# Kernel optimization log

Hardware: AMD Instinct MI355X
Metric: run time of the kernel (lower is better)

Reference implementation:

```python
import jax, jax.numpy as jnp
import numpy as np


def setup_inputs() -> dict:
    key = jax.random.key(0)
    ks = jax.random.split(key, 9)
    B, S, F = 16, 512, 1024
    scale = 1.0 / np.sqrt(2 * F)  # ~torch Linear init scale
    return {
        "v": jax.random.normal(ks[0], (B, S, F), jnp.float32),
        "t": jax.random.normal(ks[1], (B, S, F), jnp.float32),
        "a": jax.random.normal(ks[2], (B, S, F), jnp.float32),
        "W_tv": jax.random.normal(ks[3], (2 * F, F), jnp.float32) * scale,
        "b_tv": jnp.zeros((F,), jnp.float32),
        "W_ta": jax.random.normal(ks[4], (2 * F, F), jnp.float32) * scale,
        "b_ta": jnp.zeros((F,), jnp.float32),
        "W_av": jax.random.normal(ks[5], (2 * F, F), jnp.float32) * scale,
        "b_av": jnp.zeros((F,), jnp.float32),
    }


def _branch_feat(x1, x2, W, b):
    # tanh(Linear(cat(x1, x2)))  -- split weight to avoid materializing concat
    F = x1.shape[-1]
    W1, W2 = W[:F], W[F:]
    return jnp.tanh(jnp.einsum("bsf,fg->bsg", x1, W1)
                    + jnp.einsum("bsf,fg->bsg", x2, W2) + b)


def _attend_gate(q, feat):
    # softmax(q @ feat^T) @ q, gated by feat
    scores = jnp.einsum("bqf,bkf->bqk", q, feat)  # [B,S,S]
    p = jax.nn.softmax(scores, axis=-1)
    return jnp.einsum("bqk,bkf->bqf", p, q) * feat


def reference(v, t, a, W_tv, b_tv, W_ta, b_ta, W_av, b_av):
    Ftv = _branch_feat(t, v, W_tv, b_tv)
    Fta = _branch_feat(t, a, W_ta, b_ta)
    Fav = _branch_feat(a, v, W_av, b_av)
    Oatv = _attend_gate(a, Ftv)
    Ovta = _attend_gate(v, Fta)
    Otav = _attend_gate(t, Fav)
    return jnp.concatenate((Oatv, Ovta, Otav), axis=2)
```

## Files before the change

kernel.cpp:

```cpp
#include <hip/hip_runtime.h>

typedef unsigned short ushort_t;
typedef _Float16 f16x8 __attribute__((ext_vector_type(8)));
typedef float f32x4 __attribute__((ext_vector_type(4)));
typedef unsigned short u16x8 __attribute__((ext_vector_type(8)));

#define DEVINL __device__ __forceinline__

constexpr int B = 16, S = 512, F = 1024;
constexpr int M_ROWS = B * S;
constexpr size_t NX = (size_t)M_ROWS * F;
constexpr size_t NW = (size_t)F * (2 * F);

DEVINL ushort_t f2h(float f) { return __builtin_bit_cast(ushort_t, (_Float16)f); }
DEVINL float h2f(ushort_t h) { return (float)__builtin_bit_cast(_Float16, h); }

DEVINL void gload_lds16(const void* g, void* l) {
  __builtin_amdgcn_global_load_lds(
      (__attribute__((address_space(1))) void*)(g),
      (__attribute__((address_space(3))) void*)(l), 16, 0, 0);
}

DEVINL f32x4 mfma16h(f16x8 a, f16x8 b, f32x4 c) {
  return __builtin_amdgcn_mfma_f32_16x16x32_f16(a, b, c, 0, 0, 0);
}

template <int KSTEPS, int SPLIT_STEP>
DEVINL void gemm2p_core(const ushort_t* __restrict__ a1, const ushort_t* __restrict__ a2,
                        int lda, const ushort_t* __restrict__ bsrc, int ldb,
                        ushort_t* lds, int tid, f32x4 (&acc)[4][4]) {
  constexpr int BUF = 24576;
  constexpr int BOFF = 16384;
  constexpr int KM = KSTEPS - 1;
  const int lane = tid & 63, w = tid >> 6;
  const int wr = (w >> 1) * 64, wc = (w & 1) * 64;
  const int slog = (lane & 7) ^ ((lane >> 3) & 7);

  const int sl0 = ((lane >> 4) ^ (lane & 7)) * 8;
  const int sl1 = ((4 + (lane >> 4)) ^ (lane & 7)) * 8;
  const ushort_t* dsA0 = lds + (wr + (lane & 15)) * 64 + sl0;
  const ushort_t* dsA1 = lds + (wr + (lane & 15)) * 64 + sl1;
  const ushort_t* dsB0 = lds + BOFF + (wc + (lane & 15)) * 64 + sl0;
  const ushort_t* dsB1 = lds + BOFF + (wc + (lane & 15)) * 64 + sl1;

  const size_t ldaS = (size_t)lda, ldbS = (size_t)ldb;
  const ushort_t* gA1 = a1 + (size_t)(w * 16 + (lane >> 3)) * ldaS + slog * 8;
  const ushort_t* gA2 = a2 + (size_t)(w * 16 + (lane >> 3)) * ldaS + slog * 8;
  const ushort_t* gB  = bsrc + (size_t)(w * 8 + (lane >> 3)) * ldbS + slog * 8;
  ushort_t* dA = lds + (w * 16) * 64;
  ushort_t* dB = lds + BOFF + (w * 8) * 64;

  auto stA = [&](int bb, int ks, int h) {
    const ushort_t* base = ((SPLIT_STEP >= KSTEPS) || (ks < SPLIT_STEP)) ? gA1 : gA2;
    const ushort_t* s = base + (ks & (SPLIT_STEP - 1)) * 64 + (size_t)(h * 128) * ldaS;
    ushort_t* d = dA + bb * BUF + h * 8192;
    gload_lds16(s, d);
    gload_lds16(s + 8 * ldaS, d + 512);
  };
  auto stB = [&](int bb, int ks, int h) {
    const ushort_t* s = gB + ks * 64 + (size_t)(h * 64) * ldbS;
    gload_lds16(s, dB + bb * BUF + h * 4096);
  };

#define BAR asm volatile("s_barrier" ::: "memory")
#define MM2(J)                                                       \
  __builtin_amdgcn_s_setprio(1);                                     \
  _Pragma("unroll")                                                  \
  for (int i = 0; i < 4; ++i) {                                      \
    acc[i][(J)]     = mfma16h(rA[i][0], Bc0, acc[i][(J)]);           \
    acc[i][(J)]     = mfma16h(rA[i][1], Bc1, acc[i][(J)]);           \
    acc[i][(J) + 1] = mfma16h(rA[i][0], Bc2, acc[i][(J) + 1]);       \
    acc[i][(J) + 1] = mfma16h(rA[i][1], Bc3, acc[i][(J) + 1]);       \
  }                                                                  \
  __builtin_amdgcn_s_setprio(0);
#define TILE2(BB, T) {                                               \
  const int ksB = ((T) + 1) & KM;                                    \
  const int ksA = ((T) + 2) & KM;                                    \
  const ushort_t* rA0 = dsA0 + (BB) * BUF;                           \
  const ushort_t* rA1 = dsA1 + (BB) * BUF;                           \
  const ushort_t* rB0 = dsB0 + (BB) * BUF;                           \
  const ushort_t* rB1 = dsB1 + (BB) * BUF;                           \
  f16x8 rA[4][2];                                                    \
  f16x8 Bc0, Bc1, Bc2, Bc3;                                          \
  _Pragma("unroll")                                                  \
  for (int i = 0; i < 4; ++i) {                                      \
    rA[i][0] = *(const f16x8*)(rA0 + i * 1024);                      \
    rA[i][1] = *(const f16x8*)(rA1 + i * 1024);                      \
  }                                                                  \
  Bc0 = *(const f16x8*)(rB0);                                        \
  Bc1 = *(const f16x8*)(rB1);                                        \
  Bc2 = *(const f16x8*)(rB0 + 1024);                                 \
  Bc3 = *(const f16x8*)(rB1 + 1024);                                 \
  stB(BB ^ 1, ksB, 0); stB(BB ^ 1, ksB, 1);                          \
  BAR; MM2(0) BAR;                                                   \
  Bc0 = *(const f16x8*)(rB0 + 2048);                                 \
  Bc1 = *(const f16x8*)(rB1 + 2048);                                 \
  Bc2 = *(const f16x8*)(rB0 + 3072);                                 \
  Bc3 = *(const f16x8*)(rB1 + 3072);                                 \
  stA(BB, ksA, 0); stA(BB, ksA, 1);                                  \
  BAR; MM2(2)                                                        \
  asm volatile("s_waitcnt vmcnt(4)" ::: "memory");                   \
  BAR;                                                               \
}

  stA(0, 0, 0); stA(0, 0, 1);
  stB(0, 0, 0); stB(0, 0, 1);
  stA(1, 1 & KM, 0); stA(1, 1 & KM, 1);
  asm volatile("s_waitcnt vmcnt(4)" ::: "memory");
  BAR;

  for (int t = 0; t < KSTEPS; t += 2) {
    TILE2(0, t)
    TILE2(1, t + 1)
  }
#undef TILE2
#undef MM2
#undef BAR
}

__global__ __launch_bounds__(256) void split_x_kernel(
    const float* __restrict__ v, const float* __restrict__ t, const float* __restrict__ a,
    ushort_t* __restrict__ xh, ushort_t* __restrict__ xT) {
  __shared__ ushort_t tile[64][65];
  int mod = blockIdx.z;
  const float* src = (mod == 0) ? v : (mod == 1 ? t : a);
  int b = blockIdx.y;
  int s0 = (blockIdx.x >> 4) * 64;
  int f0 = (blockIdx.x & 15) * 64;
  int tid = threadIdx.x;
  ushort_t* xp = xh + mod * NX;
  ushort_t* xt = xT + mod * NX;
  int fl = (tid & 15) * 4;
#pragma unroll
  for (int r = 0; r < 4; ++r) {
    int sl = (tid >> 4) + r * 16;
    int row = b * S + s0 + sl;
    float4 x = *(const float4*)(src + (size_t)row * F + f0 + fl);
    ushort_t h0 = f2h(x.x), h1 = f2h(x.y), h2 = f2h(x.z), h3 = f2h(x.w);
    *(ushort4*)(xp + (size_t)row * F + f0 + fl) = make_ushort4(h0, h1, h2, h3);
    tile[sl][fl] = h0; tile[sl][fl + 1] = h1; tile[sl][fl + 2] = h2; tile[sl][fl + 3] = h3;
  }
  __syncthreads();
#pragma unroll
  for (int r = 0; r < 4; ++r) {
    int flr = (tid >> 4) + r * 16;
    int sl4 = (tid & 15) * 4;
    ushort4 o = make_ushort4(tile[sl4][flr], tile[sl4 + 1][flr],
                             tile[sl4 + 2][flr], tile[sl4 + 3][flr]);
    size_t tidx = ((size_t)(b * F + f0 + flr)) * S + s0 + sl4;
    *(ushort4*)(xt + tidx) = o;
  }
}

__global__ __launch_bounds__(256) void split_w_kernel(
    const float* __restrict__ w0, const float* __restrict__ w1, const float* __restrict__ w2,
    ushort_t* __restrict__ wtpack) {
  __shared__ ushort_t th[64][65];
  int br = blockIdx.z;
  const float* w = (br == 0) ? w0 : (br == 1 ? w1 : w2);
  int g0 = blockIdx.x * 64;
  int f0 = blockIdx.y * 64;
  int tid = threadIdx.x;
  int gl = (tid & 15) * 4;
#pragma unroll
  for (int r = 0; r < 4; ++r) {
    int fl = (tid >> 4) + r * 16;
    float4 x = *(const float4*)(w + (size_t)(f0 + fl) * F + g0 + gl);
    th[fl][gl] = f2h(x.x); th[fl][gl + 1] = f2h(x.y);
    th[fl][gl + 2] = f2h(x.z); th[fl][gl + 3] = f2h(x.w);
  }
  __syncthreads();
  ushort_t* op = wtpack + br * NW;
#pragma unroll
  for (int r = 0; r < 4; ++r) {
    int glr = (tid >> 4) + r * 16;
    int fl4 = (tid & 15) * 4;
    size_t o = (size_t)(g0 + glr) * (2 * F) + f0 + fl4;
    *(ushort4*)(op + o) = make_ushort4(th[fl4][glr], th[fl4 + 1][glr],
                                       th[fl4 + 2][glr], th[fl4 + 3][glr]);
  }
}

__global__ __launch_bounds__(512, 2) void feat_gemm_kernel(
    const ushort_t* __restrict__ xh, const ushort_t* __restrict__ wtpack,
    const float* __restrict__ b0, const float* __restrict__ b1, const float* __restrict__ b2,
    ushort_t* __restrict__ fpack) {
  constexpr int M1[3] = {1, 1, 2};
  constexpr int M2[3] = {0, 2, 0};
  __shared__ __attribute__((aligned(16))) ushort_t lds[2 * 24576];
  int br = blockIdx.z;
  int lin = blockIdx.x;
  int gm0 = ((lin & 7) * 4 + ((lin >> 3) & 3)) * 256;
  int gn0 = (lin >> 5) * 128;
  int tid = threadIdx.x, lane = tid & 63, w = tid >> 6;
  const ushort_t* a1 = xh + M1[br] * NX + (size_t)gm0 * F;
  const ushort_t* a2 = xh + M2[br] * NX + (size_t)gm0 * F;
  const ushort_t* bb = wtpack + br * NW + (size_t)gn0 * (2 * F);
  f32x4 acc[4][4] = {};
  gemm2p_core<32, 16>(a1, a2, F, bb, 2 * F, lds, tid, acc);
  const float* bias = (br == 0) ? b0 : (br == 1 ? b1 : b2);
  ushort_t* op = fpack + br * NX;
  int wr = (w >> 1) * 64, wc = (w & 1) * 64;
#pragma unroll
  for (int i = 0; i < 4; ++i)
#pragma unroll
    for (int j = 0; j < 4; ++j)
#pragma unroll
      for (int r = 0; r < 4; ++r) {
        int row = gm0 + wr + i * 16 + (lane >> 4) * 4 + r;
        int col = gn0 + wc + j * 16 + (lane & 15);
        op[(size_t)row * F + col] = f2h(tanhf(acc[i][j][r] + bias[col]));
      }
}

__global__ __launch_bounds__(512, 2) void attn_scores_kernel(
    const ushort_t* __restrict__ xh, const ushort_t* __restrict__ fpack,
    ushort_t* __restrict__ pbuf) {
  constexpr int QM[3] = {2, 0, 1};
  constexpr int BUFE = 20480;
  constexpr int BOFFE = 4096;
  __shared__ __attribute__((aligned(16))) ushort_t lds[3 * BUFE + 1024];
  float* redm = (float*)(lds + 3 * BUFE);
  int z = blockIdx.z;
  int br = z >> 4, b = z & 15;
  int gm0 = blockIdx.x * 128;
  int tid = threadIdx.x, lane = tid & 63, w = tid >> 6;
  int wm = w >> 2, wn = w & 3;
  int wr = wm * 64, wc = wn * 128;
  const ushort_t* qa = xh + QM[br] * NX + (size_t)(b * S + gm0) * F;
  const ushort_t* kb = fpack + br * NX + (size_t)(b * S) * F;

  const int scol = (((lane & 3) ^ ((lane >> 3) & 3)) * 8);
  const int foff = (lane & 15) * 32 + (((lane >> 4) ^ ((lane >> 1) & 3)) * 8);

  auto stA = [&](int sb, int ks) {
    const ushort_t* s = qa + (size_t)(w * 16 + (lane >> 2)) * F + ks * 32 + scol;
    gload_lds16(s, lds + sb * BUFE + w * 512);
  };
  auto stB = [&](int sb, int ks) {
#pragma unroll
    for (int g = 0; g < 4; ++g) {
      const ushort_t* s = kb + (size_t)(w * 64 + g * 16 + (lane >> 2)) * F + ks * 32 + scol;
      gload_lds16(s, lds + sb * BUFE + BOFFE + w * 2048 + g * 512);
    }
  };

  f32x4 acc[4][8] = {};
  stA(0, 0); stB(0, 0);
  stA(1, 1); stB(1, 1);
  asm volatile("s_waitcnt vmcnt(5)" ::: "memory");
  asm volatile("s_barrier" ::: "memory");

  for (int t = 0; t < 32; ++t) {
    const int cb = t % 3, sb = (t + 2) % 3;
    const int ks = (t + 2) & 31;
    stA(sb, ks); stB(sb, ks);
    const ushort_t* L = lds + cb * BUFE;
    f16x8 rA[4], rB[8];
#pragma unroll
    for (int i = 0; i < 4; ++i) rA[i] = *(const f16x8*)(L + (wr + i * 16) * 32 + foff);
#pragma unroll
    for (int j = 0; j < 8; ++j)
      rB[j] = *(const f16x8*)(L + BOFFE + (wc + j * 16) * 32 + foff);
    __builtin_amdgcn_s_setprio(1);
#pragma unroll
    for (int j = 0; j < 8; ++j)
#pragma unroll
      for (int i = 0; i < 4; ++i) acc[i][j] = mfma16h(rA[i], rB[j], acc[i][j]);
    __builtin_amdgcn_s_setprio(0);
    asm volatile("s_waitcnt vmcnt(5)" ::: "memory");
    asm volatile("s_barrier" ::: "memory");
  }

  float mx[4][4];
#pragma unroll
  for (int i = 0; i < 4; ++i)
#pragma unroll
    for (int r = 0; r < 4; ++r) {
      float m = acc[i][0][r];
#pragma unroll
      for (int j = 1; j < 8; ++j) m = fmaxf(m, acc[i][j][r]);
#pragma unroll
      for (int d = 1; d < 16; d <<= 1) m = fmaxf(m, __shfl_xor(m, d));
      mx[i][r] = m;
    }
  if ((lane & 15) == 0) {
#pragma unroll
    for (int i = 0; i < 4; ++i)
#pragma unroll
      for (int r = 0; r < 4; ++r)
        redm[wn * 128 + wr + i * 16 + (lane >> 4) * 4 + r] = mx[i][r];
  }
  __syncthreads();
  float inv[4][4];
#pragma unroll
  for (int i = 0; i < 4; ++i)
#pragma unroll
    for (int r = 0; r < 4; ++r) {
      int row = wr + i * 16 + (lane >> 4) * 4 + r;
      float fm = fmaxf(fmaxf(redm[row], redm[128 + row]),
                       fmaxf(redm[256 + row], redm[384 + row]));
      float s = 0.f;
#pragma unroll
      for (int j = 0; j < 8; ++j) {
        float e = expf(acc[i][j][r] - fm);
        acc[i][j][r] = e;
        s += e;
      }
#pragma unroll
      for (int d = 1; d < 16; d <<= 1) s += __shfl_xor(s, d);
      inv[i][r] = s;
    }
  __syncthreads();
  if ((lane & 15) == 0) {
#pragma unroll
    for (int i = 0; i < 4; ++i)
#pragma unroll
      for (int r = 0; r < 4; ++r)
        redm[wn * 128 + wr + i * 16 + (lane >> 4) * 4 + r] = inv[i][r];
  }
  __syncthreads();
  ushort_t* pout = pbuf + (size_t)z * S * S;
#pragma unroll
  for (int i = 0; i < 4; ++i)
#pragma unroll
    for (int r = 0; r < 4; ++r) {
      int row = wr + i * 16 + (lane >> 4) * 4 + r;
      float fs = (redm[row] + redm[128 + row]) + (redm[256 + row] + redm[384 + row]);
      float fi = 1.0f / fs;
#pragma unroll
      for (int j = 0; j < 8; ++j) {
        int col = wc + j * 16 + (lane & 15);
        pout[(size_t)(gm0 + row) * S + col] = f2h(acc[i][j][r] * fi);
      }
    }
}

__global__ __launch_bounds__(512, 2) void pv_gemm_kernel(
    const ushort_t* __restrict__ p, const ushort_t* __restrict__ xT,
    const ushort_t* __restrict__ fpack, float* __restrict__ out) {
  constexpr int QM[3] = {2, 0, 1};
  __shared__ __attribute__((aligned(16))) ushort_t lds[2 * 24576];
  int z = blockIdx.z;
  int br = z >> 4, b = z & 15;
  int xblk = blockIdx.x;
  int gm0 = (xblk & 1) * 256;
  int gn0 = (xblk >> 1) * 128;
  int tid = threadIdx.x, lane = tid & 63, w = tid >> 6;
  const ushort_t* pa = p + (size_t)z * S * S + (size_t)gm0 * S;
  const ushort_t* qt = xT + QM[br] * NX + (size_t)b * F * S + (size_t)gn0 * S;
  f32x4 acc[4][4] = {};
  gemm2p_core<8, 8>(pa, pa, S, qt, S, lds, tid, acc);
  const ushort_t* fp = fpack + br * NX;
  int wr = (w >> 1) * 64, wc = (w & 1) * 64;
#pragma unroll
  for (int i = 0; i < 4; ++i)
#pragma unroll
    for (int j = 0; j < 4; ++j)
#pragma unroll
      for (int r = 0; r < 4; ++r) {
        int row = gm0 + wr + i * 16 + (lane >> 4) * 4 + r;
        int col = gn0 + wc + j * 16 + (lane & 15);
        float fe = h2f(fp[(size_t)(b * S + row) * F + col]);
        out[(size_t)(b * S + row) * (3 * F) + br * F + col] = acc[i][j][r] * fe;
      }
}

extern "C" void kernel_launch(void* const* d_in, const int* in_sizes, int n_in,
                              void* d_out, int out_size, void* d_ws, size_t ws_size,
                              hipStream_t stream) {
  (void)in_sizes; (void)n_in; (void)out_size; (void)ws_size;
  const float* v = (const float*)d_in[0];
  const float* t = (const float*)d_in[1];
  const float* a = (const float*)d_in[2];
  const float* W_tv = (const float*)d_in[3];
  const float* b_tv = (const float*)d_in[4];
  const float* W_ta = (const float*)d_in[5];
  const float* b_ta = (const float*)d_in[6];
  const float* W_av = (const float*)d_in[7];
  const float* b_av = (const float*)d_in[8];
  float* out = (float*)d_out;

  ushort_t* xh = (ushort_t*)d_ws;
  ushort_t* xT = xh + 3 * NX;
  ushort_t* wtpack = xT + 3 * NX;
  ushort_t* fpack = wtpack + 3 * NW;
  ushort_t* pbuf = fpack + 3 * NX;

  split_x_kernel<<<dim3(128, 16, 3), 256, 0, stream>>>(v, t, a, xh, xT);
  split_w_kernel<<<dim3(16, 32, 3), 256, 0, stream>>>(W_tv, W_ta, W_av, wtpack);
  feat_gemm_kernel<<<dim3(256, 1, 3), 512, 0, stream>>>(xh, wtpack,
                                                        b_tv, b_ta, b_av, fpack);
  attn_scores_kernel<<<dim3(4, 1, 48), 512, 0, stream>>>(xh, fpack, pbuf);
  pv_gemm_kernel<<<dim3(16, 1, 48), 512, 0, stream>>>(pbuf, xT, fpack, out);
}
```

Measured before the change: 270.9 us.

## Load GEMM B operand directly into registers instead of staging through LDS

```diff
diff --git a/kernel.cpp b/kernel.cpp
--- a/kernel.cpp
+++ b/kernel.cpp
@@ -23,6 +23,92 @@
 
 DEVINL f32x4 mfma16h(f16x8 a, f16x8 b, f32x4 c) {
   return __builtin_amdgcn_mfma_f32_16x16x32_f16(a, b, c, 0, 0, 0);
+}
+
+template <int KSTEPS, int SPLIT_STEP>
+DEVINL void gemm_breg_core(const ushort_t* __restrict__ a1, const ushort_t* __restrict__ a2,
+                           int lda, const ushort_t* __restrict__ bsrc, int ldb,
+                           ushort_t* lds, int tid, f32x4 (&acc)[4][4]) {
+  constexpr int BUF = 16384;
+  constexpr int KM = KSTEPS - 1;
+  const int lane = tid & 63, w = tid >> 6;
+  const int wr = (w >> 1) * 64, wc = (w & 1) * 64;
+  const int slog = (lane & 7) ^ ((lane >> 3) & 7);
+
+  const int sl0 = ((lane >> 4) ^ (lane & 7)) * 8;
+  const int sl1 = ((4 + (lane >> 4)) ^ (lane & 7)) * 8;
+  const ushort_t* dsA0 = lds + (wr + (lane & 15)) * 64 + sl0;
+  const ushort_t* dsA1 = lds + (wr + (lane & 15)) * 64 + sl1;
+
+  const size_t ldaS = (size_t)lda, ldbS = (size_t)ldb;
+  const ushort_t* gA1 = a1 + (size_t)(w * 16 + (lane >> 3)) * ldaS + slog * 8;
+  const ushort_t* gA2 = a2 + (size_t)(w * 16 + (lane >> 3)) * ldaS + slog * 8;
+  ushort_t* dA = lds + (w * 16) * 64;
+
+  const ushort_t* gB = bsrc + (size_t)(wc + (lane & 15)) * ldbS + (lane >> 4) * 8;
+
+  auto stA = [&](int bb, int ks, int h) {
+    const ushort_t* base = ((SPLIT_STEP >= KSTEPS) || (ks < SPLIT_STEP)) ? gA1 : gA2;
+    const ushort_t* s = base + (ks & (SPLIT_STEP - 1)) * 64 + (size_t)(h * 128) * ldaS;
+    ushort_t* d = dA + bb * BUF + h * 8192;
+    gload_lds16(s, d);
+    gload_lds16(s + 8 * ldaS, d + 512);
+  };
+
+#define BAR asm volatile("s_barrier" ::: "memory")
+#define LDB(DST, T_) {                                               \
+  const ushort_t* gb_ = gB + (size_t)((T_) & KM) * 64;               \
+  _Pragma("unroll")                                                  \
+  for (int j = 0; j < 4; ++j) {                                      \
+    DST[j][0] = *(const f16x8*)(gb_ + (size_t)(j * 16) * ldbS);      \
+    DST[j][1] = *(const f16x8*)(gb_ + (size_t)(j * 16) * ldbS + 32); \
+  }                                                                  \
+}
+#define MMH(BC, J0)                                                  \
+  __builtin_amdgcn_s_setprio(1);                                     \
+  _Pragma("unroll")                                                  \
+  for (int i = 0; i < 4; ++i) {                                      \
+    acc[i][(J0)]     = mfma16h(rA[i][0], BC[(J0)][0], acc[i][(J0)]);         \
+    acc[i][(J0)]     = mfma16h(rA[i][1], BC[(J0)][1], acc[i][(J0)]);         \
+    acc[i][(J0) + 1] = mfma16h(rA[i][0], BC[(J0) + 1][0], acc[i][(J0) + 1]); \
+    acc[i][(J0) + 1] = mfma16h(rA[i][1], BC[(J0) + 1][1], acc[i][(J0) + 1]); \
+  }                                                                  \
+  __builtin_amdgcn_s_setprio(0);
+#define TILEB(BB, T, BCUR, BNXT) {                                   \
+  LDB(BNXT, (T) + 1)                                                 \
+  const int ksA = ((T) + 2) & KM;                                    \
+  const ushort_t* rA0 = dsA0 + (BB) * BUF;                           \
+  const ushort_t* rA1 = dsA1 + (BB) * BUF;                           \
+  f16x8 rA[4][2];                                                    \
+  _Pragma("unroll")                                                  \
+  for (int i = 0; i < 4; ++i) {                                      \
+    rA[i][0] = *(const f16x8*)(rA0 + i * 1024);                      \
+    rA[i][1] = *(const f16x8*)(rA1 + i * 1024);                      \
+  }                                                                  \
+  BAR;                                                               \
+  MMH(BCUR, 0)                                                       \
+  BAR;                                                               \
+  stA(BB, ksA, 0); stA(BB, ksA, 1);                                  \
+  MMH(BCUR, 2)                                                       \
+  asm volatile("s_waitcnt vmcnt(4)" ::: "memory");                   \
+  BAR;                                                               \
+}
+
+  f16x8 B0[4][2], B1[4][2];
+  stA(0, 0, 0); stA(0, 0, 1);
+  LDB(B0, 0)
+  stA(1, 1 & KM, 0); stA(1, 1 & KM, 1);
+  asm volatile("s_waitcnt vmcnt(4)" ::: "memory");
+  BAR;
+
+  for (int t = 0; t < KSTEPS; t += 2) {
+    TILEB(0, t, B0, B1)
+    TILEB(1, t + 1, B1, B0)
+  }
+#undef TILEB
+#undef MMH
+#undef LDB
+#undef BAR
 }
 
 template <int KSTEPS, int SPLIT_STEP>
@@ -187,7 +273,7 @@
     ushort_t* __restrict__ fpack) {
   constexpr int M1[3] = {1, 1, 2};
   constexpr int M2[3] = {0, 2, 0};
-  __shared__ __attribute__((aligned(16))) ushort_t lds[2 * 24576];
+  __shared__ __attribute__((aligned(16))) ushort_t lds[2 * 16384];
   int br = blockIdx.z;
   int lin = blockIdx.x;
   int gm0 = ((lin & 7) * 4 + ((lin >> 3) & 3)) * 256;
@@ -197,7 +283,7 @@
   const ushort_t* a2 = xh + M2[br] * NX + (size_t)gm0 * F;
   const ushort_t* bb = wtpack + br * NW + (size_t)gn0 * (2 * F);
   f32x4 acc[4][4] = {};
-  gemm2p_core<32, 16>(a1, a2, F, bb, 2 * F, lds, tid, acc);
+  gemm_breg_core<32, 16>(a1, a2, F, bb, 2 * F, lds, tid, acc);
   const float* bias = (br == 0) ? b0 : (br == 1 ? b1 : b2);
   ushort_t* op = fpack + br * NX;
   int wr = (w >> 1) * 64, wc = (w & 1) * 64;
```

Result: slower. 411.5 us (+51.9%).
